# Kernel tuning notes

Measured on AMD Instinct MI355X. Metric: run time of the kernel, lower is better.

Reference implementation:

```python
import jax, jax.numpy as jnp
import numpy as np

B = 131072
UNITS = 256
INPUT_DIM = 256


def setup_inputs() -> dict:
    key = jax.random.key(0)
    ks = jax.random.split(key, 8)
    x = jax.random.normal(ks[0], (B, INPUT_DIM), dtype=jnp.float32)
    h_prev = jax.random.normal(ks[1], (B, UNITS), dtype=jnp.float32)
    c_prev = jax.random.normal(ks[2], (B, UNITS), dtype=jnp.float32)
    # glorot-like scale for W: fan_in = INPUT_DIM + UNITS, fan_out = 4*UNITS
    scale = jnp.sqrt(2.0 / (INPUT_DIM + UNITS + 4 * UNITS)).astype(jnp.float32)
    W = jax.random.normal(ks[3], (INPUT_DIM + UNITS, 4 * UNITS), dtype=jnp.float32) * scale
    # bias: zeros except forget gate initialized to 1.0
    b = jnp.concatenate([
        jnp.zeros(UNITS, jnp.float32),
        jnp.ones(UNITS, jnp.float32),
        jnp.zeros(UNITS, jnp.float32),
        jnp.zeros(UNITS, jnp.float32),
    ])
    peephole_i = jax.random.normal(ks[4], (UNITS,), dtype=jnp.float32) * 0.05
    peephole_f = jax.random.normal(ks[5], (UNITS,), dtype=jnp.float32) * 0.05
    peephole_o = jax.random.normal(ks[6], (UNITS,), dtype=jnp.float32) * 0.05
    return {
        "x": x, "h_prev": h_prev, "c_prev": c_prev,
        "W": W, "b": b,
        "peephole_i": peephole_i, "peephole_f": peephole_f, "peephole_o": peephole_o,
    }


def reference(x, h_prev, c_prev, W, b, peephole_i, peephole_f, peephole_o):
    combined = jnp.concatenate([x, h_prev], axis=-1)          # [B, INPUT_DIM+UNITS]
    z = combined @ W + b                                      # [B, 4*UNITS]
    i, f, c_hat, o = jnp.split(z, 4, axis=1)                  # each [B, UNITS]
    i = jax.nn.sigmoid(i + peephole_i * c_prev)
    f = jax.nn.sigmoid(f + peephole_f * c_prev)
    o = jax.nn.sigmoid(o + peephole_o * c_prev)
    c_hat = jnp.tanh(c_hat)
    c = f * c_prev + i * c_hat
    h = o * jnp.tanh(c)
    return (h, h, c)  # matches (output, [h, c]) of the Keras cell
```

## Files before the change

kernel.cpp:

```cpp
#include <hip/hip_runtime.h>
#include <cstdint>

#define NROWS   131072
#define NUNITS  256
#define KTOT    512
#define BM      64
#define THREADS 256

typedef float f32x4  __attribute__((ext_vector_type(4)));
typedef short bf16x8 __attribute__((ext_vector_type(8)));

__device__ __forceinline__ short f2bf(float x) {
    unsigned u = __float_as_uint(x);
    u += 0x7FFFu + ((u >> 16) & 1u);
    return (short)(u >> 16);
}

__global__ void convert_W_kernel(const float* __restrict__ W, short* __restrict__ Wws) {
    int i = blockIdx.x * 256 + threadIdx.x;
    int k = i >> 10;
    int c = i & 1023;
    Wws[((size_t)(k >> 5) << 15) + ((size_t)c << 5) + (k & 31)] = f2bf(W[i]);
}

__global__ void __launch_bounds__(THREADS, 4)
lstm_main_kernel(const float* __restrict__ x, const float* __restrict__ h_prev,
                 const float* __restrict__ c_prev, const float* __restrict__ bias,
                 const float* __restrict__ pi, const float* __restrict__ pf,
                 const float* __restrict__ po, const short* __restrict__ Wws,
                 float* __restrict__ out) {
    __shared__ short Ab[2][2048];

    const int bid = blockIdx.x;
    const int swz = (bid & 7) * 1024 + (bid >> 3);
    const int ut  = swz & 3;
    const int rt  = swz >> 2;
    const int row0 = rt * BM;

    const int t    = threadIdx.x;
    const int lane = t & 63;
    const int w    = t >> 6;
    const int lr   = lane & 15;
    const int hi   = lane >> 4;

    const int ar = t >> 2, as_ = t & 3;
    const int avoff = ((row0 + ar) * 256 + as_ * 8) * 4;
    const int awr   = ar * 32 + ((as_ ^ ((ar >> 1) & 3)) * 8);

    const int ucol = ut * 64 + w * 16 + lr;
    const short* wfrag = Wws + ((size_t)ucol << 5) + hi * 8;

    const int sw   = (hi ^ ((lr >> 1) & 3)) * 8;
    const int aoff = lr * 32 + sw;

    f32x4 acc[4][4];
    #pragma unroll
    for (int m = 0; m < 4; ++m)
        #pragma unroll
        for (int g = 0; g < 4; ++g)
            acc[m][g] = (f32x4){0.f, 0.f, 0.f, 0.f};

    f32x4 sreg[2][2];
    auto glbA = [&](int p) {
        const char* base = (const char*)(p < 8 ? x : h_prev) + ((p & 7) << 7);
        sreg[p & 1][0] = *(const f32x4*)(base + avoff);
        sreg[p & 1][1] = *(const f32x4*)(base + avoff + 16);
    };
    auto writeA = [&](int p) {
        const f32x4* s = sreg[p & 1];
        unsigned u0_, u1_, u2_, u3_;
        asm("v_cvt_pk_bf16_f32 %0, %1, %2" : "=v"(u0_) : "v"(s[0][0]), "v"(s[0][1]));
        asm("v_cvt_pk_bf16_f32 %0, %1, %2" : "=v"(u1_) : "v"(s[0][2]), "v"(s[0][3]));
        asm("v_cvt_pk_bf16_f32 %0, %1, %2" : "=v"(u2_) : "v"(s[1][0]), "v"(s[1][1]));
        asm("v_cvt_pk_bf16_f32 %0, %1, %2" : "=v"(u3_) : "v"(s[1][2]), "v"(s[1][3]));
        int4 v = make_int4((int)u0_, (int)u1_, (int)u2_, (int)u3_);
        *(int4*)&Ab[p & 1][awr] = v;
    };

    glbA(0);
    glbA(1);
    writeA(0);
    asm volatile("s_waitcnt lgkmcnt(0)" ::: "memory");
    __builtin_amdgcn_s_barrier();

    #pragma unroll
    for (int p = 0; p < 16; ++p) {
        if (p <= 13) glbA(p + 2);

        const short* wp = wfrag + ((size_t)p << 15);
        bf16x8 bfr[4];
        #pragma unroll
        for (int g = 0; g < 4; ++g)
            bfr[g] = *(const bf16x8*)(wp + g * 8192);

        const short* A = &Ab[p & 1][0];
        bf16x8 af[4];
        #pragma unroll
        for (int m = 0; m < 4; ++m)
            af[m] = *(const bf16x8*)&A[aoff + m * 512];

        if (p <= 14) writeA(p + 1);

        __builtin_amdgcn_s_setprio(1);
        #pragma unroll
        for (int g = 0; g < 4; ++g)
            #pragma unroll
            for (int m = 0; m < 4; ++m)
                acc[m][g] = __builtin_amdgcn_mfma_f32_16x16x32_bf16(af[m], bfr[g], acc[m][g], 0, 0, 0);
        __builtin_amdgcn_s_setprio(0);

        if (p <= 14) {
            asm volatile("s_waitcnt lgkmcnt(0)" ::: "memory");
            __builtin_amdgcn_s_barrier();
        }
    }

    const size_t HS = (size_t)NROWS * NUNITS;
    const int u = ucol;
    const float bi = bias[u],       bfg = bias[256 + u];
    const float bc = bias[512 + u], bo  = bias[768 + u];
    const float ppi = pi[u], ppf = pf[u], ppo = po[u];
    #pragma unroll
    for (int m = 0; m < 4; ++m) {
        #pragma unroll
        for (int r = 0; r < 4; ++r) {
            const int row = row0 + m * 16 + hi * 4 + r;
            const size_t o = (size_t)row * NUNITS + u;
            const float cp = c_prev[o];
            float zi = acc[m][0][r] + bi  + ppi * cp;
            float zf = acc[m][1][r] + bfg + ppf * cp;
            float zc = acc[m][2][r] + bc;
            float zo = acc[m][3][r] + bo  + ppo * cp;
            float ig = 1.f / (1.f + __expf(-zi));
            float fg = 1.f / (1.f + __expf(-zf));
            float og = 1.f / (1.f + __expf(-zo));
            zc = fminf(fmaxf(zc, -30.f), 30.f);
            float e2 = __expf(2.f * zc);
            float chat = (e2 - 1.f) / (e2 + 1.f);
            float c  = fg * cp + ig * chat;
            float ccl = fminf(fmaxf(c, -30.f), 30.f);
            float e3 = __expf(2.f * ccl);
            float th = (e3 - 1.f) / (e3 + 1.f);
            float h  = og * th;
            out[o]          = h;
            out[HS + o]     = h;
            out[2 * HS + o] = c;
        }
    }
}

extern "C" void kernel_launch(void* const* d_in, const int* in_sizes, int n_in,
                              void* d_out, int out_size, void* d_ws, size_t ws_size,
                              hipStream_t stream) {
    const float* x  = (const float*)d_in[0];
    const float* h  = (const float*)d_in[1];
    const float* c  = (const float*)d_in[2];
    const float* W  = (const float*)d_in[3];
    const float* b  = (const float*)d_in[4];
    const float* pi = (const float*)d_in[5];
    const float* pf = (const float*)d_in[6];
    const float* po = (const float*)d_in[7];
    float* out = (float*)d_out;

    short* Wws = (short*)d_ws;

    hipLaunchKernelGGL(convert_W_kernel, dim3(2048), dim3(256), 0, stream, W, Wws);
    hipLaunchKernelGGL(lstm_main_kernel, dim3(NROWS / BM * 4), dim3(THREADS), 0, stream,
                       x, h, c, b, pi, pf, po, Wws, out);
}
```

Before: 314.8 us.

## Load A fragments directly from global memory, dropping LDS staging and barriers

Each wave now reads its own x/h_prev rows straight from global memory, converts them to bf16 in registers and feeds the MFMAs, replacing the shared-memory double buffer, the software prefetch and the per-step barriers. The launch-bounds occupancy hint drops from 4 to 3 blocks. This removes LDS traffic and synchronisation, but each A row is now fetched by all four waves in the block, and global-load latency is no longer hidden by the prefetch pipeline.

```diff
diff --git a/kernel.cpp b/kernel.cpp
--- a/kernel.cpp
+++ b/kernel.cpp
@@ -23,14 +23,12 @@
     Wws[((size_t)(k >> 5) << 15) + ((size_t)c << 5) + (k & 31)] = f2bf(W[i]);
 }
 
-__global__ void __launch_bounds__(THREADS, 4)
+__global__ void __launch_bounds__(THREADS, 3)
 lstm_main_kernel(const float* __restrict__ x, const float* __restrict__ h_prev,
                  const float* __restrict__ c_prev, const float* __restrict__ bias,
                  const float* __restrict__ pi, const float* __restrict__ pf,
                  const float* __restrict__ po, const short* __restrict__ Wws,
                  float* __restrict__ out) {
-    __shared__ short Ab[2][2048];
-
     const int bid = blockIdx.x;
     const int swz = (bid & 7) * 1024 + (bid >> 3);
     const int ut  = swz & 3;
@@ -43,15 +41,13 @@
     const int lr   = lane & 15;
     const int hi   = lane >> 4;
 
-    const int ar = t >> 2, as_ = t & 3;
-    const int avoff = ((row0 + ar) * 256 + as_ * 8) * 4;
-    const int awr   = ar * 32 + ((as_ ^ ((ar >> 1) & 3)) * 8);
+    int aoff[4];
+    #pragma unroll
+    for (int m = 0; m < 4; ++m)
+        aoff[m] = ((row0 + m * 16 + lr) << 10) + (hi << 5);
 
     const int ucol = ut * 64 + w * 16 + lr;
     const short* wfrag = Wws + ((size_t)ucol << 5) + hi * 8;
-
-    const int sw   = (hi ^ ((lr >> 1) & 3)) * 8;
-    const int aoff = lr * 32 + sw;
 
     f32x4 acc[4][4];
     #pragma unroll
@@ -60,32 +56,23 @@
         for (int g = 0; g < 4; ++g)
             acc[m][g] = (f32x4){0.f, 0.f, 0.f, 0.f};
 
-    f32x4 sreg[2][2];
-    auto glbA = [&](int p) {
-        const char* base = (const char*)(p < 8 ? x : h_prev) + ((p & 7) << 7);
-        sreg[p & 1][0] = *(const f32x4*)(base + avoff);
-        sreg[p & 1][1] = *(const f32x4*)(base + avoff + 16);
-    };
-    auto writeA = [&](int p) {
-        const f32x4* s = sreg[p & 1];
-        unsigned u0_, u1_, u2_, u3_;
-        asm("v_cvt_pk_bf16_f32 %0, %1, %2" : "=v"(u0_) : "v"(s[0][0]), "v"(s[0][1]));
-        asm("v_cvt_pk_bf16_f32 %0, %1, %2" : "=v"(u1_) : "v"(s[0][2]), "v"(s[0][3]));
-        asm("v_cvt_pk_bf16_f32 %0, %1, %2" : "=v"(u2_) : "v"(s[1][0]), "v"(s[1][1]));
-        asm("v_cvt_pk_bf16_f32 %0, %1, %2" : "=v"(u3_) : "v"(s[1][2]), "v"(s[1][3]));
-        int4 v = make_int4((int)u0_, (int)u1_, (int)u2_, (int)u3_);
-        *(int4*)&Ab[p & 1][awr] = v;
-    };
-
-    glbA(0);
-    glbA(1);
-    writeA(0);
-    asm volatile("s_waitcnt lgkmcnt(0)" ::: "memory");
-    __builtin_amdgcn_s_barrier();
-
     #pragma unroll
     for (int p = 0; p < 16; ++p) {
-        if (p <= 13) glbA(p + 2);
+        const char* Abase = (const char*)(p < 8 ? x : h_prev) + ((p & 7) << 7);
+
+        bf16x8 af[4];
+        #pragma unroll
+        for (int m = 0; m < 4; ++m) {
+            f32x4 lo  = *(const f32x4*)(Abase + aoff[m]);
+            f32x4 hi4 = *(const f32x4*)(Abase + aoff[m] + 16);
+            unsigned v0, v1, v2, v3;
+            asm("v_cvt_pk_bf16_f32 %0, %1, %2" : "=v"(v0) : "v"(lo[0]),  "v"(lo[1]));
+            asm("v_cvt_pk_bf16_f32 %0, %1, %2" : "=v"(v1) : "v"(lo[2]),  "v"(lo[3]));
+            asm("v_cvt_pk_bf16_f32 %0, %1, %2" : "=v"(v2) : "v"(hi4[0]), "v"(hi4[1]));
+            asm("v_cvt_pk_bf16_f32 %0, %1, %2" : "=v"(v3) : "v"(hi4[2]), "v"(hi4[3]));
+            unsigned uu[4] = {v0, v1, v2, v3};
+            af[m] = *(bf16x8*)uu;
+        }
 
         const short* wp = wfrag + ((size_t)p << 15);
         bf16x8 bfr[4];
@@ -93,26 +80,11 @@
         for (int g = 0; g < 4; ++g)
             bfr[g] = *(const bf16x8*)(wp + g * 8192);
 
-        const short* A = &Ab[p & 1][0];
-        bf16x8 af[4];
-        #pragma unroll
-        for (int m = 0; m < 4; ++m)
-            af[m] = *(const bf16x8*)&A[aoff + m * 512];
-
-        if (p <= 14) writeA(p + 1);
-
-        __builtin_amdgcn_s_setprio(1);
         #pragma unroll
         for (int g = 0; g < 4; ++g)
             #pragma unroll
             for (int m = 0; m < 4; ++m)
                 acc[m][g] = __builtin_amdgcn_mfma_f32_16x16x32_bf16(af[m], bfr[g], acc[m][g], 0, 0, 0);
-        __builtin_amdgcn_s_setprio(0);
-
-        if (p <= 14) {
-            asm volatile("s_waitcnt lgkmcnt(0)" ::: "memory");
-            __builtin_amdgcn_s_barrier();
-        }
     }
 
     const size_t HS = (size_t)NROWS * NUNITS;
```

Result: slower. 659.8 us (+109.6%).
